# Performance work log

Measured on AMD Instinct MI355X. Metric: run time of the kernel, lower is better.

The kernel has to match this reference:

```python
import jax, jax.numpy as jnp
import numpy as np

HEAD_DIM = 128
ROPE_THETA = 500000.0  # Llama3
NEG_INF = -1e9


def _apply_rope(t, cos, sin):
    # t: [b, s, h, d]; cos/sin: [s, d//2]
    b, s, h, d = t.shape
    tr = t.reshape(b, s, h, d // 2, 2)
    xr, xi = tr[..., 0], tr[..., 1]
    c = cos[None, :, None, :]
    sn = sin[None, :, None, :]
    out = jnp.stack([xr * c - xi * sn, xr * sn + xi * c], axis=-1)
    return out.reshape(b, s, h, d)


def setup_inputs() -> dict:
    key = jax.random.key(0)
    ks = jax.random.split(key, 8)
    bsz, seqlen, model_dim = 2, 2048, 4096
    n_heads, n_kv_heads, head_dim = 32, 8, HEAD_DIM
    max_bsz, max_seqlen = 2, 4096
    pos = 0

    x = jax.random.normal(ks[0], (bsz, seqlen, model_dim), dtype=jnp.float32)
    wq = jax.random.normal(ks[1], (model_dim, n_heads * head_dim), dtype=jnp.float32) * 0.02
    wk = jax.random.normal(ks[2], (model_dim, n_kv_heads * head_dim), dtype=jnp.float32) * 0.02
    wv = jax.random.normal(ks[3], (model_dim, n_kv_heads * head_dim), dtype=jnp.float32) * 0.02
    wo = jax.random.normal(ks[4], (n_heads * head_dim, model_dim), dtype=jnp.float32) * 0.02

    # RoPE tables for positions [pos, pos+seqlen)
    inv_freq = 1.0 / (ROPE_THETA ** (jnp.arange(0, head_dim, 2, dtype=jnp.float32) / head_dim))
    t = jnp.arange(pos, pos + seqlen, dtype=jnp.float32)
    ang = jnp.outer(t, inv_freq)  # [s, d//2]
    freqs_cos, freqs_sin = jnp.cos(ang), jnp.sin(ang)

    # causal additive mask over cached length (pos + seqlen)
    q_idx = jnp.arange(seqlen)[:, None] + pos
    k_idx = jnp.arange(pos + seqlen)[None, :]
    mask = jnp.where(k_idx <= q_idx, 0.0, NEG_INF).astype(jnp.float32)

    k_cache = jnp.zeros((max_bsz, max_seqlen, n_kv_heads, head_dim), dtype=jnp.float32)
    v_cache = jnp.zeros((max_bsz, max_seqlen, n_kv_heads, head_dim), dtype=jnp.float32)
    return {"x": x, "pos": pos, "freqs_cos": freqs_cos, "freqs_sin": freqs_sin,
            "mask": mask, "wq": wq, "wk": wk, "wv": wv, "wo": wo,
            "k_cache": k_cache, "v_cache": v_cache}


def reference(x, pos, freqs_cos, freqs_sin, mask, wq, wk, wv, wo, k_cache, v_cache):
    bsz, seqlen, _ = x.shape
    head_dim = 2 * freqs_cos.shape[-1]
    n_heads = wq.shape[1] // head_dim
    n_kv_heads = wk.shape[1] // head_dim

    q = (x @ wq).reshape(bsz, seqlen, n_heads, head_dim)
    k = (x @ wk).reshape(bsz, seqlen, n_kv_heads, head_dim)
    v = (x @ wv).reshape(bsz, seqlen, n_kv_heads, head_dim)

    q = _apply_rope(q, freqs_cos, freqs_sin)
    k = _apply_rope(k, freqs_cos, freqs_sin)

    # KV-cache append then read back [:, :pos+seqlen]
    k_cache = k_cache.at[:bsz, pos:pos + seqlen].set(k)
    v_cache = v_cache.at[:bsz, pos:pos + seqlen].set(v)
    keys = k_cache[:bsz, :pos + seqlen]      # [b, kv_len, n_kv, d]
    values = v_cache[:bsz, :pos + seqlen]

    repeats = n_heads // n_kv_heads
    keys = jnp.repeat(keys, repeats, axis=2)     # [b, kv_len, h, d]
    values = jnp.repeat(values, repeats, axis=2)

    scale = 1.0 / jnp.sqrt(jnp.float32(head_dim))
    scores = jnp.einsum('bqhd,bkhd->bhqk', q, keys) * scale + mask
    attn = jax.nn.softmax(scores, axis=-1)
    out = jnp.einsum('bhqk,bkhd->bqhd', attn, values)
    out = out.reshape(bsz, seqlen, n_heads * head_dim)
    return out @ wo
```

## Files before the change

### kernel.cpp

```cpp
#include <hip/hip_runtime.h>
#include <hip/hip_bf16.h>

typedef __bf16 bf16x8 __attribute__((ext_vector_type(8)));
typedef float  f32x4  __attribute__((ext_vector_type(4)));

#define DEVI __device__ __forceinline__

DEVI void async_copy16(const void* g, void* s) {
  __builtin_amdgcn_global_load_lds(
      (__attribute__((address_space(1))) void*)g,
      (__attribute__((address_space(3))) void*)s,
      16, 0, 0);
}

DEVI unsigned pack_bf16x2(float lo, float hi) {
  union { __hip_bfloat16 h[2]; unsigned u; } pk;
  pk.h[0] = __float2bfloat16(lo);
  pk.h[1] = __float2bfloat16(hi);
  return pk.u;
}

__global__ __launch_bounds__(256) void cvt_f32_bf16(const float* __restrict__ in,
                                                    __hip_bfloat16* __restrict__ out,
                                                    int n) {
  int i = (blockIdx.x * 256 + threadIdx.x) * 4;
  if (i >= n) return;
  float4 v = *(const float4*)(in + i);
  union { __hip_bfloat16 h[4]; ushort4 u; } o;
  o.h[0] = __float2bfloat16(v.x);
  o.h[1] = __float2bfloat16(v.y);
  o.h[2] = __float2bfloat16(v.z);
  o.h[3] = __float2bfloat16(v.w);
  *(ushort4*)(out + i) = o.u;
}

__global__ __launch_bounds__(256) void transpose_cvt(const float* __restrict__ W,
                                                     __hip_bfloat16* __restrict__ WT,
                                                     int Kdim, int Ndim) {
  __shared__ float tile[32][33];
  int bx = blockIdx.x * 32;
  int by = blockIdx.y * 32;
  int tx = threadIdx.x;
  int ty = threadIdx.y;
  #pragma unroll
  for (int j = 0; j < 32; j += 8)
    tile[ty + j][tx] = W[(size_t)(by + ty + j) * Ndim + bx + tx];
  __syncthreads();
  #pragma unroll
  for (int j = 0; j < 32; j += 8)
    WT[(size_t)(bx + ty + j) * Kdim + by + tx] = __float2bfloat16(tile[tx][ty + j]);
}

__global__ __launch_bounds__(256) void transpose_v(const __hip_bfloat16* __restrict__ vb,
                                                   __hip_bfloat16* __restrict__ vt) {
  __shared__ __hip_bfloat16 tile[32][33];
  const int s0 = blockIdx.x * 32, d0 = blockIdx.y * 32;
  const int bk = blockIdx.z;
  const int bb = bk >> 3, kvh = bk & 7;
  const int tx = threadIdx.x, ty = threadIdx.y;
  #pragma unroll
  for (int j = 0; j < 32; j += 8)
    tile[ty + j][tx] =
        vb[((size_t)(bb * 2048 + s0 + ty + j) * 8 + kvh) * 128 + d0 + tx];
  __syncthreads();
  #pragma unroll
  for (int j = 0; j < 32; j += 8)
    vt[((size_t)bk * 128 + d0 + ty + j) * 2048 + s0 + tx] = tile[tx][ty + j];
}

template <int EPI>
__global__ __launch_bounds__(512, 2) void gemm256(
    const __hip_bfloat16* __restrict__ A,
    const __hip_bfloat16* __restrict__ BT,
    float* __restrict__ Cf,
    __hip_bfloat16* __restrict__ Cb,
    int M, int N, int K,
    const float* __restrict__ fcos,
    const float* __restrict__ fsin,
    float scale) {
  __shared__ alignas(16) char lds[2][65536];
  const int tid = threadIdx.x;
  const int w = tid >> 6, l = tid & 63;
  const int l4 = l >> 4, l15 = l & 15;
  const int wr = w >> 2, wc = w & 3;
  const int rowBase = blockIdx.y * 256;
  const int colBase = blockIdx.x * 256;

  const __hip_bfloat16* aS[2];
  const __hip_bfloat16* bS[2];
  int dstOff[2];
  #pragma unroll
  for (int i = 0; i < 2; i++) {
    int c = i * 512 + tid;
    int r = c >> 3;
    int kb = (c & 7) ^ (r & 7);
    aS[i] = A  + (size_t)(rowBase + r) * K + kb * 8;
    bS[i] = BT + (size_t)(colBase + r) * K + kb * 8;
    dstOff[i] = i * 8192 + w * 1024;
  }
  const size_t hstep = (size_t)128 * K;

  f32x4 acc[8][4];
  #pragma unroll
  for (int mi = 0; mi < 8; mi++)
    #pragma unroll
    for (int ni = 0; ni < 4; ni++)
      acc[mi][ni] = (f32x4){0.f, 0.f, 0.f, 0.f};

  #pragma unroll
  for (int i = 0; i < 2; i++) async_copy16(aS[i],         lds[0] + 0     + dstOff[i]);
  #pragma unroll
  for (int i = 0; i < 2; i++) async_copy16(aS[i] + hstep, lds[0] + 16384 + dstOff[i]);
  #pragma unroll
  for (int i = 0; i < 2; i++) async_copy16(bS[i],         lds[0] + 32768 + dstOff[i]);
  #pragma unroll
  for (int i = 0; i < 2; i++) async_copy16(bS[i] + hstep, lds[0] + 49152 + dstOff[i]);

  const int NT = K >> 6;
  const int pswz = l15 & 7;
  bf16x8 bF[4][2];

  for (int kt = 0; kt < NT; kt++) {
    const char* bufc = lds[kt & 1];
    char* bufn = lds[(kt & 1) ^ 1];
    const int koff = (kt + 1) * 64;
    const bool pre = (kt + 1 < NT);

    if (pre) {
      #pragma unroll
      for (int i = 0; i < 2; i++) async_copy16(aS[i] + koff, bufn + 0 + dstOff[i]);
    }
    if (pre) { asm volatile("s_waitcnt vmcnt(2)" ::: "memory"); }
    else     { asm volatile("s_waitcnt vmcnt(0)" ::: "memory"); }
    __builtin_amdgcn_s_barrier();
    __builtin_amdgcn_sched_barrier(0);

    #pragma unroll
    for (int ni = 0; ni < 4; ni++)
      #pragma unroll
      for (int kh = 0; kh < 2; kh++) {
        int R = wc * 64 + ni * 16 + l15;
        int phys = (kh * 4 + l4) ^ pswz;
        bF[ni][kh] = *(const bf16x8*)(bufc + 32768 + (R >> 7) * 16384 +
                                      (R & 127) * 128 + phys * 16);
      }
    {
      bf16x8 aF[2][2];
      #pragma unroll
      for (int f = 0; f < 2; f++)
        #pragma unroll
        for (int kh = 0; kh < 2; kh++) {
          int lr = f * 16 + l15;
          int phys = (kh * 4 + l4) ^ pswz;
          aF[f][kh] = *(const bf16x8*)(bufc + wr * 16384 + lr * 128 + phys * 16);
        }
      asm volatile("s_waitcnt lgkmcnt(0)" ::: "memory");
      __builtin_amdgcn_sched_barrier(0);
      __builtin_amdgcn_s_setprio(1);
      #pragma unroll
      for (int f = 0; f < 2; f++)
        #pragma unroll
        for (int ni = 0; ni < 4; ni++)
          #pragma unroll
          for (int kh = 0; kh < 2; kh++)
            acc[f][ni] = __builtin_amdgcn_mfma_f32_16x16x32_bf16(
                aF[f][kh], bF[ni][kh], acc[f][ni], 0, 0, 0);
      __builtin_amdgcn_s_setprio(0);
    }
    __builtin_amdgcn_s_barrier();

    #pragma unroll
    for (int p = 1; p < 4; p++) {
      bf16x8 aF[2][2];
      #pragma unroll
      for (int f = 0; f < 2; f++)
        #pragma unroll
        for (int kh = 0; kh < 2; kh++) {
          int lr = (2 * p + f) * 16 + l15;
          int phys = (kh * 4 + l4) ^ pswz;
          aF[f][kh] = *(const bf16x8*)(bufc + wr * 16384 + lr * 128 + phys * 16);
        }
      if (pre) {
        if (p == 1) {
          #pragma unroll
          for (int i = 0; i < 2; i++)
            async_copy16(aS[i] + hstep + koff, bufn + 16384 + dstOff[i]);
        } else if (p == 2) {
          #pragma unroll
          for (int i = 0; i < 2; i++)
            async_copy16(bS[i] + koff, bufn + 32768 + dstOff[i]);
        } else {
          #pragma unroll
          for (int i = 0; i < 2; i++)
            async_copy16(bS[i] + hstep + koff, bufn + 49152 + dstOff[i]);
        }
      }
      __builtin_amdgcn_s_barrier();
      asm volatile("s_waitcnt lgkmcnt(0)" ::: "memory");
      __builtin_amdgcn_sched_barrier(0);
      __builtin_amdgcn_s_setprio(1);
      #pragma unroll
      for (int f = 0; f < 2; f++)
        #pragma unroll
        for (int ni = 0; ni < 4; ni++)
          #pragma unroll
          for (int kh = 0; kh < 2; kh++)
            acc[2 * p + f][ni] = __builtin_amdgcn_mfma_f32_16x16x32_bf16(
                aF[f][kh], bF[ni][kh], acc[2 * p + f][ni], 0, 0, 0);
      __builtin_amdgcn_s_setprio(0);
      __builtin_amdgcn_s_barrier();
    }
  }

  const int orow0 = rowBase + wr * 128 + l4 * 4;
  const int ocol0 = colBase + wc * 64 + l15;
  #pragma unroll
  for (int mi = 0; mi < 8; mi++) {
    #pragma unroll
    for (int ni = 0; ni < 4; ni++) {
      #pragma unroll
      for (int reg = 0; reg < 4; reg++) {
        int r = orow0 + mi * 16 + reg;
        int col = ocol0 + ni * 16;
        float v = acc[mi][ni][reg];
        if constexpr (EPI == 0) {
          Cf[(size_t)r * N + col] = v;
        } else {
          float p2 = __shfl_xor(v, 1);
          int dd = col & 127;
          int fi = dd >> 1;
          int srow = r & 2047;
          float c = fcos[srow * 64 + fi];
          float s = fsin[srow * 64 + fi];
          float outv = ((col & 1) == 0) ? (v * c - p2 * s) : (p2 * s + v * c);
          Cb[(size_t)r * N + col] = __float2bfloat16(outv * scale);
        }
      }
    }
  }
}

template <int EPI>
__global__ __launch_bounds__(256) void gemm_bt(
    const __hip_bfloat16* __restrict__ A,
    const __hip_bfloat16* __restrict__ BT,
    float* __restrict__ Cf,
    __hip_bfloat16* __restrict__ Cb,
    __hip_bfloat16* __restrict__ Cb2,
    int M, int N, int K,
    const float* __restrict__ fcos,
    const float* __restrict__ fsin,
    float scale) {
  __shared__ alignas(16) __hip_bfloat16 lds[3][8192];
  const int tid = threadIdx.x;
  const int w = tid >> 6, l = tid & 63;
  const int l4 = l >> 4, l15 = l & 15;
  const int wr = w >> 1, wc = w & 1;
  const int rowBase = blockIdx.y * 128;
  const int colBase = blockIdx.x * 128;

  const __hip_bfloat16* aSrc[2];
  const __hip_bfloat16* bSrc[2];
  int dstOff[2];
  #pragma unroll
  for (int i = 0; i < 2; i++) {
    int c = i * 256 + tid;
    int r = c >> 2;
    int kb = (c & 3) ^ ((r >> 1) & 3);
    aSrc[i] = A  + (size_t)(rowBase + r) * K + kb * 8;
    bSrc[i] = BT + (size_t)(colBase + r) * K + kb * 8;
    dstOff[i] = (i * 256 + w * 64) * 16;
  }

  f32x4 acc[4][4];
  #pragma unroll
  for (int mi = 0; mi < 4; mi++)
    #pragma unroll
    for (int ni = 0; ni < 4; ni++)
      acc[mi][ni] = (f32x4){0.f, 0.f, 0.f, 0.f};

  #pragma unroll
  for (int i = 0; i < 2; i++) {
    async_copy16(aSrc[i], (char*)lds + dstOff[i]);
    async_copy16(bSrc[i], (char*)lds + 8192 + dstOff[i]);
  }
  #pragma unroll
  for (int i = 0; i < 2; i++) {
    async_copy16(aSrc[i] + 32, (char*)lds + 16384 + dstOff[i]);
    async_copy16(bSrc[i] + 32, (char*)lds + 16384 + 8192 + dstOff[i]);
  }

  int cur = 0;
  for (int k0 = 0; k0 < K; k0 += 32) {
    if (k0 + 32 < K) {
      asm volatile("s_waitcnt vmcnt(4)" ::: "memory");
    } else {
      asm volatile("s_waitcnt vmcnt(0)" ::: "memory");
    }
    __builtin_amdgcn_s_barrier();
    __builtin_amdgcn_sched_barrier(0);

    const char* base = (const char*)lds + cur * 16384;
    bf16x8 aF[4], bF[4];
    #pragma unroll
    for (int mi = 0; mi < 4; mi++) {
      int row = wr * 64 + mi * 16 + l15;
      int phys = l4 ^ ((row >> 1) & 3);
      aF[mi] = *(const bf16x8*)(base + row * 64 + phys * 16);
    }
    #pragma unroll
    for (int ni = 0; ni < 4; ni++) {
      int row = wc * 64 + ni * 16 + l15;
      int phys = l4 ^ ((row >> 1) & 3);
      bF[ni] = *(const bf16x8*)(base + 8192 + row * 64 + phys * 16);
    }
    asm volatile("s_waitcnt lgkmcnt(0)" ::: "memory");
    __builtin_amdgcn_sched_barrier(0);

    if (k0 + 64 < K) {
      int nxt = cur + 2; if (nxt >= 3) nxt -= 3;
      #pragma unroll
      for (int i = 0; i < 2; i++) {
        async_copy16(aSrc[i] + k0 + 64, (char*)lds + nxt * 16384 + dstOff[i]);
        async_copy16(bSrc[i] + k0 + 64, (char*)lds + nxt * 16384 + 8192 + dstOff[i]);
      }
    }

    __builtin_amdgcn_s_setprio(1);
    #pragma unroll
    for (int mi = 0; mi < 4; mi++)
      #pragma unroll
      for (int ni = 0; ni < 4; ni++)
        acc[mi][ni] = __builtin_amdgcn_mfma_f32_16x16x32_bf16(aF[mi], bF[ni], acc[mi][ni], 0, 0, 0);
    __builtin_amdgcn_s_setprio(0);
    cur = (cur + 1 == 3) ? 0 : cur + 1;
  }

  const int orow0 = rowBase + wr * 64 + l4 * 4;
  const int ocol0 = colBase + wc * 64 + l15;
  #pragma unroll
  for (int mi = 0; mi < 4; mi++) {
    #pragma unroll
    for (int ni = 0; ni < 4; ni++) {
      #pragma unroll
      for (int reg = 0; reg < 4; reg++) {
        int r = orow0 + mi * 16 + reg;
        int col = ocol0 + ni * 16;
        float v = acc[mi][ni][reg];
        if constexpr (EPI == 0) {
          Cf[(size_t)r * N + col] = v;
        } else if constexpr (EPI == 1) {
          Cb[(size_t)r * N + col] = __float2bfloat16(v * scale);
        } else if constexpr (EPI == 2) {
          float p = __shfl_xor(v, 1);
          int dd = col & 127;
          int fi = dd >> 1;
          int srow = r & 2047;
          float c = fcos[srow * 64 + fi];
          float s = fsin[srow * 64 + fi];
          float outv = ((col & 1) == 0) ? (v * c - p * s) : (p * s + v * c);
          Cb[(size_t)r * N + col] = __float2bfloat16(outv * scale);
        } else {
          if (colBase < 1024) {
            float p = __shfl_xor(v, 1);
            int dd = col & 127;
            int fi = dd >> 1;
            int srow = r & 2047;
            float c = fcos[srow * 64 + fi];
            float s = fsin[srow * 64 + fi];
            float outv = ((col & 1) == 0) ? (v * c - p * s) : (p * s + v * c);
            Cb[(size_t)r * 1024 + col] = __float2bfloat16(outv);
          } else {
            Cb2[(size_t)r * 1024 + (col - 1024)] = __float2bfloat16(v);
          }
        }
      }
    }
  }
}

__global__ __launch_bounds__(256, 2) void attn_kernel(
    const __hip_bfloat16* __restrict__ Q,
    const __hip_bfloat16* __restrict__ Kb,
    const __hip_bfloat16* __restrict__ Vt_g,
    __hip_bfloat16* __restrict__ O) {
  const int S = 2048, HD = 4096, KVD = 1024, D = 128;
  const int h = blockIdx.y, b = blockIdx.z;
  const int kvh = h >> 2;
  const int bk = b * 8 + kvh;
  const int tid = threadIdx.x;
  const int w = tid >> 6, l = tid & 63;
  const int l4 = l >> 4, l15 = l & 15;

  __shared__ alignas(16) __hip_bfloat16 Kt[2][64 * 128];
  __shared__ alignas(16) __hip_bfloat16 Vt[2][128 * 64];
  __shared__ alignas(16) __hip_bfloat16 Pb[4 * 32 * 64];

  const __hip_bfloat16* kSrc[4];
  const __hip_bfloat16* vSrc[4];
  int stDst[4];
  #pragma unroll
  for (int i = 0; i < 4; i++) {
    int c = i * 256 + tid;
    int kr = c >> 4;
    int kds = (c & 15) ^ (kr & 7);
    kSrc[i] = Kb + (size_t)(b * S + kr) * KVD + kvh * D + kds * 8;
    int vr = c >> 3;
    int vds = (c & 7) ^ (vr & 7);
    vSrc[i] = Vt_g + ((size_t)bk * 128 + vr) * 2048 + vds * 8;
    stDst[i] = (i * 256 + w * 64) * 16;
  }

  char* pbase = (char*)Pb + w * 4096;

  for (int pass = 0; pass < 2; pass++) {
    const int qt = pass ? (15 - blockIdx.x) : blockIdx.x;
    const int qbase = qt * 128 + w * 32;
    const int nt = 2 * qt + 2;

    bf16x8 qf[2][4];
    #pragma unroll
    for (int f = 0; f < 2; f++) {
      const int qrow = qbase + f * 16 + l15;
      const __hip_bfloat16* qptr = Q + (size_t)(b * S + qrow) * HD + h * D + l4 * 8;
      #pragma unroll
      for (int dc = 0; dc < 4; dc++) qf[f][dc] = *(const bf16x8*)(qptr + dc * 32);
    }

    f32x4 o[2][8];
    #pragma unroll
    for (int f = 0; f < 2; f++)
      #pragma unroll
      for (int nf = 0; nf < 8; nf++) o[f][nf] = (f32x4){0.f, 0.f, 0.f, 0.f};
    float mrun[2]  = {-1e30f, -1e30f};
    float llrun[2] = {0.f, 0.f};

    if (pass) __syncthreads();

    #pragma unroll
    for (int i = 0; i < 4; i++) {
      async_copy16(kSrc[i], (char*)Kt + stDst[i]);
      async_copy16(vSrc[i], (char*)Vt + stDst[i]);
    }

    int cur = 0;
    for (int t = 0; t < nt; t++) {
      __syncthreads();
      if (t + 1 < nt) {
        const int kv1 = (t + 1) * 64;
        #pragma unroll
        for (int i = 0; i < 4; i++) {
          async_copy16(kSrc[i] + (size_t)kv1 * KVD, (char*)Kt + (cur ^ 1) * 16384 + stDst[i]);
          async_copy16(vSrc[i] + kv1,               (char*)Vt + (cur ^ 1) * 16384 + stDst[i]);
        }
      }
      const char* ktb = (const char*)Kt + cur * 16384;
      const char* vtb = (const char*)Vt + cur * 16384;
      const int kv0 = t * 64;

      f32x4 s[2][4];
      #pragma unroll
      for (int f = 0; f < 2; f++)
        #pragma unroll
        for (int kg = 0; kg < 4; kg++) s[f][kg] = (f32x4){0.f, 0.f, 0.f, 0.f};
      __builtin_amdgcn_s_setprio(1);
      #pragma unroll
      for (int dc = 0; dc < 4; dc++) {
        #pragma unroll
        for (int kg = 0; kg < 4; kg++) {
          int key = kg * 16 + l15;
          int phys = (dc * 4 + l4) ^ (key & 7);
          bf16x8 kf = *(const bf16x8*)(ktb + key * 256 + phys * 16);
          s[0][kg] = __builtin_amdgcn_mfma_f32_16x16x32_bf16(kf, qf[0][dc], s[0][kg], 0, 0, 0);
          s[1][kg] = __builtin_amdgcn_mfma_f32_16x16x32_bf16(kf, qf[1][dc], s[1][kg], 0, 0, 0);
        }
      }
      __builtin_amdgcn_s_setprio(0);

      if (t >= nt - 2) {
        #pragma unroll
        for (int f = 0; f < 2; f++) {
          int q = qbase + f * 16 + l15;
          #pragma unroll
          for (int kg = 0; kg < 4; kg++)
            #pragma unroll
            for (int reg = 0; reg < 4; reg++)
              if (kv0 + kg * 16 + 4 * l4 + reg > q) s[f][kg][reg] = -1e30f;
        }
      }

      #pragma unroll
      for (int f = 0; f < 2; f++) {
        float pmax = -1e30f;
        #pragma unroll
        for (int kg = 0; kg < 4; kg++)
          #pragma unroll
          for (int reg = 0; reg < 4; reg++) pmax = fmaxf(pmax, s[f][kg][reg]);
        pmax = fmaxf(pmax, __shfl_xor(pmax, 16));
        pmax = fmaxf(pmax, __shfl_xor(pmax, 32));
        float mn = fmaxf(mrun[f], pmax);
        float alpha = __expf(mrun[f] - mn);
        mrun[f] = mn;
        float rs = 0.f;
        #pragma unroll
        for (int kg = 0; kg < 4; kg++)
          #pragma unroll
          for (int reg = 0; reg < 4; reg++) {
            float p = __expf(s[f][kg][reg] - mn);
            s[f][kg][reg] = p;
            rs += p;
          }
        rs += __shfl_xor(rs, 16);
        rs += __shfl_xor(rs, 32);
        llrun[f] = llrun[f] * alpha + rs;

        #pragma unroll
        for (int kg = 0; kg < 4; kg++)
          #pragma unroll
          for (int p2 = 0; p2 < 2; p2++) {
            unsigned u = pack_bf16x2(s[f][kg][2 * p2], s[f][kg][2 * p2 + 1]);
            int slot16 = 2 * kg + (l4 >> 1);
            int inner = (8 * l4 + 4 * p2) & 15;
            *(unsigned*)(pbase + (f * 16 + l15) * 128 + ((slot16 ^ (l15 & 7)) * 16) + inner) = u;
          }

        float alpha_r[4];
        #pragma unroll
        for (int reg = 0; reg < 4; reg++)
          alpha_r[reg] = __shfl(alpha, (l & 48) + 4 * l4 + reg);
        #pragma unroll
        for (int nf = 0; nf < 8; nf++)
          #pragma unroll
          for (int reg = 0; reg < 4; reg++) o[f][nf][reg] *= alpha_r[reg];
      }

      __builtin_amdgcn_s_setprio(1);
      #pragma unroll
      for (int half = 0; half < 2; half++) {
        int physp = (half * 4 + l4) ^ (l15 & 7);
        bf16x8 pa0 = *(const bf16x8*)(pbase + (0 * 16 + l15) * 128 + physp * 16);
        bf16x8 pa1 = *(const bf16x8*)(pbase + (1 * 16 + l15) * 128 + physp * 16);
        #pragma unroll
        for (int nf = 0; nf < 8; nf++) {
          int d = nf * 16 + l15;
          bf16x8 vf = *(const bf16x8*)(vtb + d * 128 + physp * 16);
          o[0][nf] = __builtin_amdgcn_mfma_f32_16x16x32_bf16(pa0, vf, o[0][nf], 0, 0, 0);
          o[1][nf] = __builtin_amdgcn_mfma_f32_16x16x32_bf16(pa1, vf, o[1][nf], 0, 0, 0);
        }
      }
      __builtin_amdgcn_s_setprio(0);
      cur ^= 1;
    }

    #pragma unroll
    for (int f = 0; f < 2; f++) {
      #pragma unroll
      for (int reg = 0; reg < 4; reg++) {
        float llr = __shfl(llrun[f], (l & 48) + 4 * l4 + reg);
        float inv = 1.0f / llr;
        int r = qbase + f * 16 + 4 * l4 + reg;
        __hip_bfloat16* optr = O + (size_t)(b * S + r) * HD + h * D + l15;
        #pragma unroll
        for (int nf = 0; nf < 8; nf++) optr[nf * 16] = __float2bfloat16(o[f][nf][reg] * inv);
      }
    }
  }
}

extern "C" void kernel_launch(void* const* d_in, const int* in_sizes, int n_in,
                              void* d_out, int out_size, void* d_ws, size_t ws_size,
                              hipStream_t stream) {
  const float* x    = (const float*)d_in[0];
  const float* fcos = (const float*)d_in[2];
  const float* fsin = (const float*)d_in[3];
  const float* wq   = (const float*)d_in[5];
  const float* wk   = (const float*)d_in[6];
  const float* wv   = (const float*)d_in[7];
  const float* wo   = (const float*)d_in[8];
  float* out = (float*)d_out;

  char* ws = (char*)d_ws;
  const size_t MB = 1024 * 1024;
  __hip_bfloat16* xb  = (__hip_bfloat16*)(ws + 0);
  __hip_bfloat16* wT  = (__hip_bfloat16*)(ws + 32 * MB);
  __hip_bfloat16* wkT = (__hip_bfloat16*)(ws + 64 * MB);
  __hip_bfloat16* wvT = (__hip_bfloat16*)(ws + 72 * MB);
  __hip_bfloat16* qb  = (__hip_bfloat16*)(ws + 80 * MB);
  __hip_bfloat16* kb  = (__hip_bfloat16*)(ws + 112 * MB);
  __hip_bfloat16* vb  = (__hip_bfloat16*)(ws + 120 * MB);
  __hip_bfloat16* ab  = xb;
  __hip_bfloat16* vt  = wT;

  const float qscale = 0.08838834764831845f;

  cvt_f32_bf16<<<16384, 256, 0, stream>>>(x, xb, 16777216);
  transpose_cvt<<<dim3(128, 128), dim3(32, 8), 0, stream>>>(wq, wT, 4096, 4096);
  transpose_cvt<<<dim3(32, 128), dim3(32, 8), 0, stream>>>(wk, wkT, 4096, 1024);
  transpose_cvt<<<dim3(32, 128), dim3(32, 8), 0, stream>>>(wv, wvT, 4096, 1024);

  gemm256<2><<<dim3(16, 16), 512, 0, stream>>>(xb, wT, nullptr, qb,
                                               4096, 4096, 4096, fcos, fsin, qscale);
  gemm_bt<3><<<dim3(16, 32), 256, 0, stream>>>(xb, wkT, nullptr, kb, vb,
                                               4096, 2048, 4096, fcos, fsin, 1.0f);

  transpose_v<<<dim3(64, 4, 16), dim3(32, 8), 0, stream>>>(vb, vt);

  attn_kernel<<<dim3(8, 32, 2), 256, 0, stream>>>(qb, kb, vt, ab);

  transpose_cvt<<<dim3(128, 128), dim3(32, 8), 0, stream>>>(wo, wT, 4096, 4096);
  gemm256<0><<<dim3(16, 16), 512, 0, stream>>>(ab, wT, out, nullptr,
                                               4096, 4096, 4096, nullptr, nullptr, 1.0f);
}
```

Baseline: 514.4 us.

## Fuse Q, K and V projections into one 256-tile GEMM launch

Drops the separate 128-tile K/V GEMM kernel. The Q, K and V projections now run as a single gemm256 launch with N=6144. This relies on the transposed wq, wk and wv buffers sitting next to each other in the workspace, and splits the epilogue by column range: Q gets RoPE and the scale, K gets RoPE only, V is stored unchanged. The goal is to remove one launch and fill the GPU with one larger grid of big tiles instead of two smaller ones. The change also moves the B-fragment LDS reads after the A reads and removes the explicit lgkmcnt waits and sched barriers, so the compiler now places the LDS waits and schedules the loads.

```diff
diff --git a/kernel.cpp b/kernel.cpp
--- a/kernel.cpp
+++ b/kernel.cpp
@@ -74,6 +74,8 @@
     const __hip_bfloat16* __restrict__ BT,
     float* __restrict__ Cf,
     __hip_bfloat16* __restrict__ Cb,
+    __hip_bfloat16* __restrict__ Cb2,
+    __hip_bfloat16* __restrict__ Cb3,
     int M, int N, int K,
     const float* __restrict__ fcos,
     const float* __restrict__ fsin,
@@ -133,17 +135,7 @@
     if (pre) { asm volatile("s_waitcnt vmcnt(2)" ::: "memory"); }
     else     { asm volatile("s_waitcnt vmcnt(0)" ::: "memory"); }
     __builtin_amdgcn_s_barrier();
-    __builtin_amdgcn_sched_barrier(0);
-
-    #pragma unroll
-    for (int ni = 0; ni < 4; ni++)
-      #pragma unroll
-      for (int kh = 0; kh < 2; kh++) {
-        int R = wc * 64 + ni * 16 + l15;
-        int phys = (kh * 4 + l4) ^ pswz;
-        bF[ni][kh] = *(const bf16x8*)(bufc + 32768 + (R >> 7) * 16384 +
-                                      (R & 127) * 128 + phys * 16);
-      }
+
     {
       bf16x8 aF[2][2];
       #pragma unroll
@@ -154,8 +146,15 @@
           int phys = (kh * 4 + l4) ^ pswz;
           aF[f][kh] = *(const bf16x8*)(bufc + wr * 16384 + lr * 128 + phys * 16);
         }
-      asm volatile("s_waitcnt lgkmcnt(0)" ::: "memory");
-      __builtin_amdgcn_sched_barrier(0);
+      #pragma unroll
+      for (int ni = 0; ni < 4; ni++)
+        #pragma unroll
+        for (int kh = 0; kh < 2; kh++) {
+          int R = wc * 64 + ni * 16 + l15;
+          int phys = (kh * 4 + l4) ^ pswz;
+          bF[ni][kh] = *(const bf16x8*)(bufc + 32768 + (R >> 7) * 16384 +
+                                        (R & 127) * 128 + phys * 16);
+        }
       __builtin_amdgcn_s_setprio(1);
       #pragma unroll
       for (int f = 0; f < 2; f++)
@@ -196,8 +195,6 @@
         }
       }
       __builtin_amdgcn_s_barrier();
-      asm volatile("s_waitcnt lgkmcnt(0)" ::: "memory");
-      __builtin_amdgcn_sched_barrier(0);
       __builtin_amdgcn_s_setprio(1);
       #pragma unroll
       for (int f = 0; f < 2; f++)
@@ -226,152 +223,24 @@
         if constexpr (EPI == 0) {
           Cf[(size_t)r * N + col] = v;
         } else {
-          float p2 = __shfl_xor(v, 1);
-          int dd = col & 127;
-          int fi = dd >> 1;
-          int srow = r & 2047;
-          float c = fcos[srow * 64 + fi];
-          float s = fsin[srow * 64 + fi];
-          float outv = ((col & 1) == 0) ? (v * c - p2 * s) : (p2 * s + v * c);
-          Cb[(size_t)r * N + col] = __float2bfloat16(outv * scale);
-        }
-      }
-    }
-  }
-}
-
-template <int EPI>
-__global__ __launch_bounds__(256) void gemm_bt(
-    const __hip_bfloat16* __restrict__ A,
-    const __hip_bfloat16* __restrict__ BT,
-    float* __restrict__ Cf,
-    __hip_bfloat16* __restrict__ Cb,
-    __hip_bfloat16* __restrict__ Cb2,
-    int M, int N, int K,
-    const float* __restrict__ fcos,
-    const float* __restrict__ fsin,
-    float scale) {
-  __shared__ alignas(16) __hip_bfloat16 lds[3][8192];
-  const int tid = threadIdx.x;
-  const int w = tid >> 6, l = tid & 63;
-  const int l4 = l >> 4, l15 = l & 15;
-  const int wr = w >> 1, wc = w & 1;
-  const int rowBase = blockIdx.y * 128;
-  const int colBase = blockIdx.x * 128;
-
-  const __hip_bfloat16* aSrc[2];
-  const __hip_bfloat16* bSrc[2];
-  int dstOff[2];
-  #pragma unroll
-  for (int i = 0; i < 2; i++) {
-    int c = i * 256 + tid;
-    int r = c >> 2;
-    int kb = (c & 3) ^ ((r >> 1) & 3);
-    aSrc[i] = A  + (size_t)(rowBase + r) * K + kb * 8;
-    bSrc[i] = BT + (size_t)(colBase + r) * K + kb * 8;
-    dstOff[i] = (i * 256 + w * 64) * 16;
-  }
-
-  f32x4 acc[4][4];
-  #pragma unroll
-  for (int mi = 0; mi < 4; mi++)
-    #pragma unroll
-    for (int ni = 0; ni < 4; ni++)
-      acc[mi][ni] = (f32x4){0.f, 0.f, 0.f, 0.f};
-
-  #pragma unroll
-  for (int i = 0; i < 2; i++) {
-    async_copy16(aSrc[i], (char*)lds + dstOff[i]);
-    async_copy16(bSrc[i], (char*)lds + 8192 + dstOff[i]);
-  }
-  #pragma unroll
-  for (int i = 0; i < 2; i++) {
-    async_copy16(aSrc[i] + 32, (char*)lds + 16384 + dstOff[i]);
-    async_copy16(bSrc[i] + 32, (char*)lds + 16384 + 8192 + dstOff[i]);
-  }
-
-  int cur = 0;
-  for (int k0 = 0; k0 < K; k0 += 32) {
-    if (k0 + 32 < K) {
-      asm volatile("s_waitcnt vmcnt(4)" ::: "memory");
-    } else {
-      asm volatile("s_waitcnt vmcnt(0)" ::: "memory");
-    }
-    __builtin_amdgcn_s_barrier();
-    __builtin_amdgcn_sched_barrier(0);
-
-    const char* base = (const char*)lds + cur * 16384;
-    bf16x8 aF[4], bF[4];
-    #pragma unroll
-    for (int mi = 0; mi < 4; mi++) {
-      int row = wr * 64 + mi * 16 + l15;
-      int phys = l4 ^ ((row >> 1) & 3);
-      aF[mi] = *(const bf16x8*)(base + row * 64 + phys * 16);
-    }
-    #pragma unroll
-    for (int ni = 0; ni < 4; ni++) {
-      int row = wc * 64 + ni * 16 + l15;
-      int phys = l4 ^ ((row >> 1) & 3);
-      bF[ni] = *(const bf16x8*)(base + 8192 + row * 64 + phys * 16);
-    }
-    asm volatile("s_waitcnt lgkmcnt(0)" ::: "memory");
-    __builtin_amdgcn_sched_barrier(0);
-
-    if (k0 + 64 < K) {
-      int nxt = cur + 2; if (nxt >= 3) nxt -= 3;
-      #pragma unroll
-      for (int i = 0; i < 2; i++) {
-        async_copy16(aSrc[i] + k0 + 64, (char*)lds + nxt * 16384 + dstOff[i]);
-        async_copy16(bSrc[i] + k0 + 64, (char*)lds + nxt * 16384 + 8192 + dstOff[i]);
-      }
-    }
-
-    __builtin_amdgcn_s_setprio(1);
-    #pragma unroll
-    for (int mi = 0; mi < 4; mi++)
-      #pragma unroll
-      for (int ni = 0; ni < 4; ni++)
-        acc[mi][ni] = __builtin_amdgcn_mfma_f32_16x16x32_bf16(aF[mi], bF[ni], acc[mi][ni], 0, 0, 0);
-    __builtin_amdgcn_s_setprio(0);
-    cur = (cur + 1 == 3) ? 0 : cur + 1;
-  }
-
-  const int orow0 = rowBase + wr * 64 + l4 * 4;
-  const int ocol0 = colBase + wc * 64 + l15;
-  #pragma unroll
-  for (int mi = 0; mi < 4; mi++) {
-    #pragma unroll
-    for (int ni = 0; ni < 4; ni++) {
-      #pragma unroll
-      for (int reg = 0; reg < 4; reg++) {
-        int r = orow0 + mi * 16 + reg;
-        int col = ocol0 + ni * 16;
-        float v = acc[mi][ni][reg];
-        if constexpr (EPI == 0) {
-          Cf[(size_t)r * N + col] = v;
-        } else if constexpr (EPI == 1) {
-          Cb[(size_t)r * N + col] = __float2bfloat16(v * scale);
-        } else if constexpr (EPI == 2) {
-          float p = __shfl_xor(v, 1);
-          int dd = col & 127;
-          int fi = dd >> 1;
-          int srow = r & 2047;
-          float c = fcos[srow * 64 + fi];
-          float s = fsin[srow * 64 + fi];
-          float outv = ((col & 1) == 0) ? (v * c - p * s) : (p * s + v * c);
-          Cb[(size_t)r * N + col] = __float2bfloat16(outv * scale);
-        } else {
-          if (colBase < 1024) {
-            float p = __shfl_xor(v, 1);
-            int dd = col & 127;
-            int fi = dd >> 1;
+          if (colBase < 4096) {
+            float p2 = __shfl_xor(v, 1);
+            int fi = (col & 127) >> 1;
             int srow = r & 2047;
             float c = fcos[srow * 64 + fi];
             float s = fsin[srow * 64 + fi];
-            float outv = ((col & 1) == 0) ? (v * c - p * s) : (p * s + v * c);
-            Cb[(size_t)r * 1024 + col] = __float2bfloat16(outv);
+            float outv = ((col & 1) == 0) ? (v * c - p2 * s) : (p2 * s + v * c);
+            Cb[(size_t)r * 4096 + col] = __float2bfloat16(outv * scale);
+          } else if (colBase < 5120) {
+            float p2 = __shfl_xor(v, 1);
+            int fi = (col & 127) >> 1;
+            int srow = r & 2047;
+            float c = fcos[srow * 64 + fi];
+            float s = fsin[srow * 64 + fi];
+            float outv = ((col & 1) == 0) ? (v * c - p2 * s) : (p2 * s + v * c);
+            Cb2[(size_t)r * 1024 + (col - 4096)] = __float2bfloat16(outv);
           } else {
-            Cb2[(size_t)r * 1024 + (col - 1024)] = __float2bfloat16(v);
+            Cb3[(size_t)r * 1024 + (col - 5120)] = __float2bfloat16(v);
           }
         }
       }
@@ -598,16 +467,14 @@
   transpose_cvt<<<dim3(32, 128), dim3(32, 8), 0, stream>>>(wk, wkT, 4096, 1024);
   transpose_cvt<<<dim3(32, 128), dim3(32, 8), 0, stream>>>(wv, wvT, 4096, 1024);
 
-  gemm256<2><<<dim3(16, 16), 512, 0, stream>>>(xb, wT, nullptr, qb,
-                                               4096, 4096, 4096, fcos, fsin, qscale);
-  gemm_bt<3><<<dim3(16, 32), 256, 0, stream>>>(xb, wkT, nullptr, kb, vb,
-                                               4096, 2048, 4096, fcos, fsin, 1.0f);
+  gemm256<4><<<dim3(24, 16), 512, 0, stream>>>(xb, wT, nullptr, qb, kb, vb,
+                                               4096, 6144, 4096, fcos, fsin, qscale);
 
   transpose_v<<<dim3(64, 4, 16), dim3(32, 8), 0, stream>>>(vb, vt);
 
   attn_kernel<<<dim3(8, 32, 2), 256, 0, stream>>>(qb, kb, vt, ab);
 
   transpose_cvt<<<dim3(128, 128), dim3(32, 8), 0, stream>>>(wo, wT, 4096, 4096);
-  gemm256<0><<<dim3(16, 16), 512, 0, stream>>>(ab, wT, out, nullptr,
+  gemm256<0><<<dim3(16, 16), 512, 0, stream>>>(ab, wT, out, nullptr, nullptr, nullptr,
                                                4096, 4096, 4096, nullptr, nullptr, 1.0f);
 }
```

Result: slower. 561.2 us (+9.1%).
